# Optimization experiments

Hardware: AMD Instinct MI355X
Metric: run time of the kernel (lower is better)

Reference implementation:

```python
import jax, jax.numpy as jnp
import numpy as np

N_NODES = 79
RAW_FEAT = 26
D_IN = RAW_FEAT + 6      # 32, in_channels after position concat
D_OUT = 2 * D_IN         # 64, out_channel_fac * in_channels
HIDDEN = 256
N_EDGES = 3000
BATCH = 256
POS_IDX = [120,124,128,132,136,140,144,148,152,237,241,245,249,253,257,261,265,269,354,358,362,366,370,374,378,382,386,471,475,479,483,487,491,495,499,503,588,592,596,600,604,608,612,616,620,705,709,713,717,721,725,729,733,737,822,826,830,834,838,842,846,850,854,48,53,60,67,73,157,352,388,583,586,817,901,906,913,920,926]


def _positions():
    width, height = 39, 25
    p = np.asarray(POS_IDX)
    xn = (p % width) / (width - 1)
    yn = (p // width) / (height - 1)
    feats = np.stack([xn, yn,
                      (np.sin(xn * 2 * np.pi) + 1) / 2,
                      (np.cos(xn * 2 * np.pi) + 1) / 2,
                      (np.sin(yn * 2 * np.pi) + 1) / 2,
                      (np.cos(yn * 2 * np.pi) + 1) / 2], axis=-1)
    return jnp.asarray(feats, jnp.float32)


def setup_inputs() -> dict:
    key = jax.random.key(0)
    ks = jax.random.split(key, 20)
    s = 0.05
    inp = {
        "state": jax.random.normal(ks[0], (BATCH, N_NODES, RAW_FEAT), jnp.float32),
        "pos_feat": _positions(),
        "edge_weights": jax.random.uniform(ks[1], (N_EDGES, 1), jnp.float32),
        # TransformerConv params (heads=1, edge_dim=1): torch Linear weights [out,in]
        "Wq": jax.random.normal(ks[2], (D_OUT, D_IN)) * s, "bq": jnp.zeros((D_OUT,)),
        "Wk": jax.random.normal(ks[3], (D_OUT, D_IN)) * s, "bk": jnp.zeros((D_OUT,)),
        "Wv": jax.random.normal(ks[4], (D_OUT, D_IN)) * s, "bv": jnp.zeros((D_OUT,)),
        "We": jax.random.normal(ks[5], (D_OUT, 1)) * s,            # lin_edge, bias=False
        "Wskip": jax.random.normal(ks[6], (D_OUT, D_IN)) * s, "bskip": jnp.zeros((D_OUT,)),
        # MLP head
        "W1": jax.random.normal(ks[7], (HIDDEN, D_IN + D_OUT + 1)) * s, "b1": jnp.zeros((HIDDEN,)),
        "g1": jnp.ones((HIDDEN,)), "beta1": jnp.zeros((HIDDEN,)),
        "W2": jax.random.normal(ks[8], (HIDDEN, HIDDEN)) * s, "b2": jnp.zeros((HIDDEN,)),
        "g2": jnp.ones((HIDDEN,)), "beta2": jnp.zeros((HIDDEN,)),
        "W3": jax.random.normal(ks[9], (1, HIDDEN)) * s, "b3": jnp.zeros((1,)),
        "edge_index": jax.random.randint(ks[10], (2, N_EDGES), 0, N_NODES, jnp.int32),
    }
    return inp


def _layernorm(x, g, b):
    m = x.mean(-1, keepdims=True)
    v = ((x - m) ** 2).mean(-1, keepdims=True)
    return (x - m) / jnp.sqrt(v + 1e-5) * g + b


def reference(state, pos_feat, edge_weights, Wq, bq, Wk, bk, Wv, bv, We, Wskip, bskip,
              W1, b1, g1, beta1, W2, b2, g2, beta2, W3, b3, edge_index):
    B = state.shape[0]
    # concat normalized positional features (shared across batch)
    x = jnp.concatenate([state, jnp.broadcast_to(pos_feat, (B, N_NODES, 6))], -1)  # [B,N,D_IN]
    src, dst = edge_index[0], edge_index[1]
    e = edge_weights @ We.T  # [E, D_OUT] edge embedding, shared across batch
    scale = 1.0 / jnp.sqrt(jnp.float32(D_OUT))

    def conv_one(xg):  # TransformerConv, heads=1, concat, root_weight
        q = xg @ Wq.T + bq
        k = xg @ Wk.T + bk
        v = xg @ Wv.T + bv
        ke = k[src] + e                      # [E, D_OUT]
        ve = v[src] + e
        alpha = (q[dst] * ke).sum(-1) * scale  # [E]
        amax = jax.ops.segment_max(alpha, dst, num_segments=N_NODES)
        amax = jnp.where(jnp.isfinite(amax), amax, 0.0)
        ex = jnp.exp(alpha - amax[dst])
        den = jax.ops.segment_sum(ex, dst, num_segments=N_NODES)
        w = ex / (den[dst] + 1e-16)
        agg = jax.ops.segment_sum(ve * w[:, None], dst, num_segments=N_NODES)
        return agg + xg @ Wskip.T + bskip

    out1 = jax.nn.relu(jax.vmap(conv_one)(x))  # [B,N,D_OUT]
    total_agents = x[..., 1].sum(-1)[:, None, None]  # [B,1,1]
    h = jnp.concatenate([out1, jnp.broadcast_to(total_agents, (B, N_NODES, 1)), x], -1)
    h = jax.nn.leaky_relu(_layernorm(h @ W1.T + b1, g1, beta1))
    h = jax.nn.leaky_relu(_layernorm(h @ W2.T + b2, g2, beta2))
    conc = jax.nn.softplus(h @ W3.T + b3).squeeze(-1)  # [B,N]
    action = conc / (conc.sum(-1, keepdims=True) + 1e-20)  # deterministic path
    return action
```

## Files before the change

### kernel.cpp

```cpp
#include <hip/hip_runtime.h>
#include <hip/hip_bf16.h>

#define N_NODES 79
#define RAW_FEAT 26
#define D_IN 32
#define D_OUT 64
#define HIDDEN 256
#define N_EDGES 3000
#define BATCH 256
#define M_ROWS (BATCH * N_NODES)
#define K1PAD 112

__global__ __launch_bounds__(256) void k_prep(
    const float* __restrict__ W1, const float* __restrict__ W2,
    const int* __restrict__ ei, const float* __restrict__ ew,
    float* __restrict__ W1t, float* __restrict__ W2t,
    int* __restrict__ rp, int* __restrict__ csr_src,
    int* __restrict__ csr_dst, float* __restrict__ csr_ew)
{
    __shared__ float tile[64][65];
    __shared__ int cnt[N_NODES];
    __shared__ int base[N_NODES + 1];
    const int tid = threadIdx.x, bid = blockIdx.x;

    if (bid < 24) {
        const float* in; float* out; int C, Kpad, kb, rb;
        if (bid < 8) { in = W1; out = W1t; C = 97; Kpad = K1PAD;
                       kb = (bid & 1) * 64; rb = (bid >> 1) * 64; }
        else         { int b = bid - 8; in = W2; out = W2t; C = 256; Kpad = 256;
                       kb = (b & 3) * 64; rb = (b >> 2) * 64; }
        for (int i = tid; i < 4096; i += 256) {
            int rr = i >> 6, kk = i & 63;
            int r = rb + rr, k = kb + kk;
            tile[rr][kk] = (k < C) ? in[r * C + k] : 0.f;
        }
        __syncthreads();
        for (int i = tid; i < 4096; i += 256) {
            int kk = i >> 6, rr = i & 63;
            int k = kb + kk, r = rb + rr;
            if (k < Kpad) out[(size_t)k * HIDDEN + r] = tile[rr][kk];
        }
        return;
    }

    if (tid < N_NODES) cnt[tid] = 0;
    __syncthreads();
    for (int e = tid; e < N_EDGES; e += 256) atomicAdd(&cnt[ei[N_EDGES + e]], 1);
    __syncthreads();
    if (tid == 0) {
        int run = 0;
        for (int n = 0; n < N_NODES; ++n) { base[n] = run; run += cnt[n]; }
        base[N_NODES] = run;
    }
    __syncthreads();
    if (tid < N_NODES + 1) rp[tid] = base[tid];
    if (tid < N_NODES) cnt[tid] = base[tid];
    __syncthreads();
    for (int e = tid; e < N_EDGES; e += 256) {
        int d = ei[N_EDGES + e];
        int p = atomicAdd(&cnt[d], 1);
        csr_src[p] = ei[e];
        csr_dst[p] = d;
        csr_ew[p]  = ew[e];
    }
}

#define DOT4(S, Aa, Bb) S += Aa.x * Bb.x + Aa.y * Bb.y + Aa.z * Bb.z + Aa.w * Bb.w;

__global__ __launch_bounds__(512) void k1_conv(
    const float* __restrict__ state, const float* __restrict__ pos,
    const int* __restrict__ rp_g, const int* __restrict__ csrc_g,
    const int* __restrict__ cdst_g, const float* __restrict__ cew_g,
    const float* __restrict__ Wq, const float* __restrict__ bq,
    const float* __restrict__ Wk, const float* __restrict__ bk,
    const float* __restrict__ Wv, const float* __restrict__ bv,
    const float* __restrict__ We, const float* __restrict__ Wsk,
    const float* __restrict__ bsk,
    float* __restrict__ out1_ws, float* __restrict__ ta_ws)
{
    __shared__ __align__(16) float qs [80 * 68];
    __shared__ __align__(16) float kss[80 * 68];
    __shared__ __align__(16) float vss[80 * 68];
    __shared__ __align__(16) float o1s[N_NODES * 68];
    __shared__ __align__(16) float xs[N_NODES * 32];
    __shared__ __align__(16) float SA[80 * 80];
    __shared__ __align__(16) float alpha[N_EDGES];
    __shared__ __align__(16) float ewc[N_EDGES];
    __shared__ unsigned short srcs[N_EDGES], dsts[N_EDGES];
    __shared__ __align__(16) float eW[64];
    __shared__ int   rp_s[80];
    __shared__ float qWe[80], csum_s[80];

    const int b = blockIdx.x, tid = threadIdx.x;

    for (int t = tid; t < N_NODES * 32; t += 512) {
        int n = t >> 5, c = t & 31;
        xs[t] = (c < RAW_FEAT) ? state[(b * N_NODES + n) * RAW_FEAT + c]
                               : pos[n * 6 + (c - RAW_FEAT)];
    }
    for (int t = tid; t < N_EDGES; t += 512) {
        srcs[t] = (unsigned short)csrc_g[t];
        dsts[t] = (unsigned short)cdst_g[t];
        ewc[t]  = cew_g[t];
    }
    if (tid < 64) eW[tid] = We[tid];
    if (tid < 80) rp_s[tid] = rp_g[tid];
    for (int t = tid; t < 68; t += 512) {
        qs[79 * 68 + t] = 0.f; kss[79 * 68 + t] = 0.f; vss[79 * 68 + t] = 0.f;
    }
    __syncthreads();

    {
        const float4* xs4 = (const float4*)xs;
        const float4* Wq4 = (const float4*)Wq;
        const float4* Wk4 = (const float4*)Wk;
        const float4* Wv4 = (const float4*)Wv;
        const float4* Ws4 = (const float4*)Wsk;
        for (int t = tid; t < N_NODES * 64; t += 512) {
            int n = t >> 6, d = t & 63;
            float aq = bq[d], ak = bk[d], av = bv[d], ask = bsk[d];
            #pragma unroll
            for (int c4 = 0; c4 < 8; ++c4) {
                float4 xv = xs4[n * 8 + c4];
                float4 wq = Wq4[d * 8 + c4];
                float4 wk = Wk4[d * 8 + c4];
                float4 wv = Wv4[d * 8 + c4];
                float4 wsv = Ws4[d * 8 + c4];
                DOT4(aq, xv, wq)
                DOT4(ak, xv, wk)
                DOT4(av, xv, wv)
                DOT4(ask, xv, wsv)
            }
            qs [n * 68 + d] = aq;
            kss[n * 68 + d] = ak;
            vss[n * 68 + d] = av;
            o1s[n * 68 + d] = ask;
        }
        if (tid == 511) {
            float s = 0.f;
            #pragma unroll
            for (int n = 0; n < N_NODES; ++n) s += xs[n * 32 + 1];
            ta_ws[b] = s;
        }
    }
    __syncthreads();

    if (tid < N_NODES) {
        const float4* q4 = (const float4*)(qs + tid * 68);
        const float4* e4 = (const float4*)eW;
        float s = 0.f;
        #pragma unroll
        for (int i = 0; i < 16; ++i) {
            float4 a = q4[i], e = e4[i];
            DOT4(s, a, e)
        }
        qWe[tid] = s;
    }
    __syncthreads();

    {
        const int rg = tid >> 5, cgp = tid & 31;
        const int r0 = rg * 5;
        int c0 = cgp * 3; if (c0 > 76) c0 = 76;
        float s00 = 0, s01 = 0, s02 = 0;
        float s10 = 0, s11 = 0, s12 = 0;
        float s20 = 0, s21 = 0, s22 = 0;
        float s30 = 0, s31 = 0, s32 = 0;
        float s40 = 0, s41 = 0, s42 = 0;
        const float4* q4p = (const float4*)qs;
        const float4* k4p = (const float4*)kss;
        for (int k4 = 0; k4 < 16; ++k4) {
            float4 q0 = q4p[(r0 + 0) * 17 + k4];
            float4 q1 = q4p[(r0 + 1) * 17 + k4];
            float4 q2 = q4p[(r0 + 2) * 17 + k4];
            float4 q3 = q4p[(r0 + 3) * 17 + k4];
            float4 q4v = q4p[(r0 + 4) * 17 + k4];
            float4 c0v = k4p[(c0 + 0) * 17 + k4];
            float4 c1v = k4p[(c0 + 1) * 17 + k4];
            float4 c2v = k4p[(c0 + 2) * 17 + k4];
            DOT4(s00, q0, c0v)  DOT4(s01, q0, c1v)  DOT4(s02, q0, c2v)
            DOT4(s10, q1, c0v)  DOT4(s11, q1, c1v)  DOT4(s12, q1, c2v)
            DOT4(s20, q2, c0v)  DOT4(s21, q2, c1v)  DOT4(s22, q2, c2v)
            DOT4(s30, q3, c0v)  DOT4(s31, q3, c1v)  DOT4(s32, q3, c2v)
            DOT4(s40, q4v, c0v) DOT4(s41, q4v, c1v) DOT4(s42, q4v, c2v)
        }
        SA[(r0 + 0) * 80 + c0 + 0] = s00; SA[(r0 + 0) * 80 + c0 + 1] = s01; SA[(r0 + 0) * 80 + c0 + 2] = s02;
        SA[(r0 + 1) * 80 + c0 + 0] = s10; SA[(r0 + 1) * 80 + c0 + 1] = s11; SA[(r0 + 1) * 80 + c0 + 2] = s12;
        SA[(r0 + 2) * 80 + c0 + 0] = s20; SA[(r0 + 2) * 80 + c0 + 1] = s21; SA[(r0 + 2) * 80 + c0 + 2] = s22;
        SA[(r0 + 3) * 80 + c0 + 0] = s30; SA[(r0 + 3) * 80 + c0 + 1] = s31; SA[(r0 + 3) * 80 + c0 + 2] = s32;
        SA[(r0 + 4) * 80 + c0 + 0] = s40; SA[(r0 + 4) * 80 + c0 + 1] = s41; SA[(r0 + 4) * 80 + c0 + 2] = s42;
    }
    __syncthreads();

    for (int t = tid; t < N_EDGES; t += 512) {
        int s = srcs[t], d = dsts[t];
        alpha[t] = 0.125f * (SA[d * 80 + s] + ewc[t] * qWe[d]);
    }
    __syncthreads();

    for (int t = tid; t < 6400; t += 512) SA[t] = 0.f;
    __syncthreads();

    if (tid < N_NODES) {
        int e0 = rp_s[tid], e1 = rp_s[tid + 1];
        float m = -1e30f;
        for (int e = e0; e < e1; ++e) m = fmaxf(m, alpha[e]);
        float s = 0.f, cs = 0.f;
        for (int e = e0; e < e1; ++e) {
            float ex = expf(alpha[e] - m);
            alpha[e] = ex;
            s += ex; cs += ex * ewc[e];
        }
        float rden = 1.f / (s + 1e-16f);
        csum_s[tid] = cs * rden;
        float* Ar = SA + tid * 80;
        for (int e = e0; e < e1; ++e) Ar[srcs[e]] += alpha[e] * rden;
    }
    __syncthreads();

    {
        const int rowg = tid >> 4, colg = tid & 15;
        int n0 = rowg * 3; if (n0 > 76) n0 = 76;
        float4 g0 = {0.f, 0.f, 0.f, 0.f};
        float4 g1 = {0.f, 0.f, 0.f, 0.f};
        float4 g2 = {0.f, 0.f, 0.f, 0.f};
        const float4* A4  = (const float4*)SA;
        const float4* v4p = (const float4*)vss;

#define AGGSTEP(COMP, SS) { \
        float4 vv = v4p[(s4 * 4 + SS) * 17 + colg]; \
        g0.x += a0.COMP * vv.x; g0.y += a0.COMP * vv.y; g0.z += a0.COMP * vv.z; g0.w += a0.COMP * vv.w; \
        g1.x += a1.COMP * vv.x; g1.y += a1.COMP * vv.y; g1.z += a1.COMP * vv.z; g1.w += a1.COMP * vv.w; \
        g2.x += a2.COMP * vv.x; g2.y += a2.COMP * vv.y; g2.z += a2.COMP * vv.z; g2.w += a2.COMP * vv.w; }

        for (int s4 = 0; s4 < 20; ++s4) {
            float4 a0 = A4[(n0 + 0) * 20 + s4];
            float4 a1 = A4[(n0 + 1) * 20 + s4];
            float4 a2 = A4[(n0 + 2) * 20 + s4];
            AGGSTEP(x, 0)
            AGGSTEP(y, 1)
            AGGSTEP(z, 2)
            AGGSTEP(w, 3)
        }
#undef AGGSTEP

        const float4* o4 = (const float4*)o1s;
        const float4* e4 = (const float4*)eW;
        float4 ev = e4[colg];

#define AGGOUT(GI, I) { int n = n0 + I; if (n < N_NODES) { \
        float4 sk = o4[n * 17 + colg]; float cs = csum_s[n]; float4 r; \
        r.x = fmaxf(sk.x + GI.x + cs * ev.x, 0.f); \
        r.y = fmaxf(sk.y + GI.y + cs * ev.y, 0.f); \
        r.z = fmaxf(sk.z + GI.z + cs * ev.z, 0.f); \
        r.w = fmaxf(sk.w + GI.w + cs * ev.w, 0.f); \
        ((float4*)out1_ws)[((size_t)b * N_NODES + n) * 16 + colg] = r; } }

        AGGOUT(g0, 0)
        AGGOUT(g1, 1)
        AGGOUT(g2, 2)
#undef AGGOUT
    }
}

__global__ __launch_bounds__(256, 4) void k23_mlp(
    const float* __restrict__ state, const float* __restrict__ pos,
    const float* __restrict__ out1_ws, const float* __restrict__ ta_ws,
    const float* __restrict__ W1t, const float* __restrict__ b1,
    const float* __restrict__ g1, const float* __restrict__ be1,
    const float* __restrict__ W2t, const float* __restrict__ b2,
    const float* __restrict__ g2, const float* __restrict__ be2,
    const float* __restrict__ W3, const float* __restrict__ b3,
    float* __restrict__ conc_ws)
{
    __shared__ __align__(16) float A1[16 * K1PAD];
    __shared__ __align__(16) float A2[16 * 256];
    __shared__ __align__(16) float Ws[16 * 256];

    const int tid = threadIdx.x;
    const int lane = tid & 63;
    const int wv = tid >> 6;
    const int m0 = blockIdx.x * 16;

    const float4* W1t4 = (const float4*)W1t;
    const float4* W2t4 = (const float4*)W2t;
    const float4* A1r4 = (const float4*)A1;
    const float4* A2r4 = (const float4*)A2;
    float4* Ws4 = (float4*)Ws;
    const float4* Wsc4 = (const float4*)Ws;

    for (int t = tid; t < 16 * K1PAD; t += 256) {
        int r = t / K1PAD, k = t - r * K1PAD;
        int m = m0 + r;
        float v = 0.f;
        if (k < 64)       v = out1_ws[m * 64 + k];
        else if (k == 64) v = ta_ws[m / N_NODES];
        else if (k < 91)  v = state[m * RAW_FEAT + (k - 65)];
        else if (k < 97)  { int n = m - (m / N_NODES) * N_NODES;
                            v = pos[n * 6 + (k - 91)]; }
        A1[t] = v;
    }

    float4 pre0 = W1t4[(wv + 0) * 64 + lane];
    float4 pre1 = W1t4[(wv + 4) * 64 + lane];
    float4 pre2 = W1t4[(wv + 8) * 64 + lane];
    float4 pre3 = W1t4[(wv + 12) * 64 + lane];
    __syncthreads();

    float4 acc0 = {0.f, 0.f, 0.f, 0.f};
    float4 acc1 = {0.f, 0.f, 0.f, 0.f};
    float4 acc2 = {0.f, 0.f, 0.f, 0.f};
    float4 acc3 = {0.f, 0.f, 0.f, 0.f};

#define GSTEP(COMP, WIDX) { \
    float4 w = Wsc4[(kq * 4 + WIDX) * 64 + lane]; \
    acc0.x += a0.COMP * w.x; acc0.y += a0.COMP * w.y; acc0.z += a0.COMP * w.z; acc0.w += a0.COMP * w.w; \
    acc1.x += a1.COMP * w.x; acc1.y += a1.COMP * w.y; acc1.z += a1.COMP * w.z; acc1.w += a1.COMP * w.w; \
    acc2.x += a2.COMP * w.x; acc2.y += a2.COMP * w.y; acc2.z += a2.COMP * w.z; acc2.w += a2.COMP * w.w; \
    acc3.x += a3.COMP * w.x; acc3.y += a3.COMP * w.y; acc3.z += a3.COMP * w.z; acc3.w += a3.COMP * w.w; }

    for (int ch = 0; ch < 7; ++ch) {
        Ws4[(wv + 0) * 64 + lane] = pre0;
        Ws4[(wv + 4) * 64 + lane] = pre1;
        Ws4[(wv + 8) * 64 + lane] = pre2;
        Ws4[(wv + 12) * 64 + lane] = pre3;
        __syncthreads();
        if (ch < 6) {
            pre0 = W1t4[((ch + 1) * 16 + wv + 0) * 64 + lane];
            pre1 = W1t4[((ch + 1) * 16 + wv + 4) * 64 + lane];
            pre2 = W1t4[((ch + 1) * 16 + wv + 8) * 64 + lane];
            pre3 = W1t4[((ch + 1) * 16 + wv + 12) * 64 + lane];
        }
        #pragma unroll
        for (int kq = 0; kq < 4; ++kq) {
            float4 a0 = A1r4[(4 * wv + 0) * 28 + ch * 4 + kq];
            float4 a1 = A1r4[(4 * wv + 1) * 28 + ch * 4 + kq];
            float4 a2 = A1r4[(4 * wv + 2) * 28 + ch * 4 + kq];
            float4 a3 = A1r4[(4 * wv + 3) * 28 + ch * 4 + kq];
            GSTEP(x, 0)
            GSTEP(y, 1)
            GSTEP(z, 2)
            GSTEP(w, 3)
        }
        __syncthreads();
    }

    pre0 = W2t4[(wv + 0) * 64 + lane];
    pre1 = W2t4[(wv + 4) * 64 + lane];
    pre2 = W2t4[(wv + 8) * 64 + lane];
    pre3 = W2t4[(wv + 12) * 64 + lane];

    {
        float4 bv = ((const float4*)b1)[lane];
        float4 gv = ((const float4*)g1)[lane];
        float4 ev = ((const float4*)be1)[lane];

#define LN1_ROW(ACC, RR) { \
        float v0 = ACC.x + bv.x, v1 = ACC.y + bv.y, v2 = ACC.z + bv.z, v3 = ACC.w + bv.w; \
        float sm = v0 + v1 + v2 + v3, sq = v0 * v0 + v1 * v1 + v2 * v2 + v3 * v3; \
        for (int off = 32; off >= 1; off >>= 1) { sm += __shfl_xor(sm, off, 64); sq += __shfl_xor(sq, off, 64); } \
        float mu = sm * (1.f / 256.f), rstd = rsqrtf(sq * (1.f / 256.f) - mu * mu + 1e-5f); \
        float4 yv; \
        yv.x = (v0 - mu) * rstd * gv.x + ev.x; yv.y = (v1 - mu) * rstd * gv.y + ev.y; \
        yv.z = (v2 - mu) * rstd * gv.z + ev.z; yv.w = (v3 - mu) * rstd * gv.w + ev.w; \
        yv.x = yv.x > 0.f ? yv.x : 0.01f * yv.x; yv.y = yv.y > 0.f ? yv.y : 0.01f * yv.y; \
        yv.z = yv.z > 0.f ? yv.z : 0.01f * yv.z; yv.w = yv.w > 0.f ? yv.w : 0.01f * yv.w; \
        ((float4*)A2)[(4 * wv + RR) * 64 + lane] = yv; }

        LN1_ROW(acc0, 0)
        LN1_ROW(acc1, 1)
        LN1_ROW(acc2, 2)
        LN1_ROW(acc3, 3)
#undef LN1_ROW
        acc0 = {0.f, 0.f, 0.f, 0.f};
        acc1 = {0.f, 0.f, 0.f, 0.f};
        acc2 = {0.f, 0.f, 0.f, 0.f};
        acc3 = {0.f, 0.f, 0.f, 0.f};
    }
    __syncthreads();

    for (int ch = 0; ch < 16; ++ch) {
        Ws4[(wv + 0) * 64 + lane] = pre0;
        Ws4[(wv + 4) * 64 + lane] = pre1;
        Ws4[(wv + 8) * 64 + lane] = pre2;
        Ws4[(wv + 12) * 64 + lane] = pre3;
        __syncthreads();
        if (ch < 15) {
            pre0 = W2t4[((ch + 1) * 16 + wv + 0) * 64 + lane];
            pre1 = W2t4[((ch + 1) * 16 + wv + 4) * 64 + lane];
            pre2 = W2t4[((ch + 1) * 16 + wv + 8) * 64 + lane];
            pre3 = W2t4[((ch + 1) * 16 + wv + 12) * 64 + lane];
        }
        #pragma unroll
        for (int kq = 0; kq < 4; ++kq) {
            float4 a0 = A2r4[(4 * wv + 0) * 64 + ch * 4 + kq];
            float4 a1 = A2r4[(4 * wv + 1) * 64 + ch * 4 + kq];
            float4 a2 = A2r4[(4 * wv + 2) * 64 + ch * 4 + kq];
            float4 a3 = A2r4[(4 * wv + 3) * 64 + ch * 4 + kq];
            GSTEP(x, 0)
            GSTEP(y, 1)
            GSTEP(z, 2)
            GSTEP(w, 3)
        }
        __syncthreads();
    }
#undef GSTEP

    {
        float4 bv = ((const float4*)b2)[lane];
        float4 gv = ((const float4*)g2)[lane];
        float4 ev = ((const float4*)be2)[lane];
        float4 w3 = ((const float4*)W3)[lane];
        float bb3 = b3[0];

#define LN2_ROW(ACC, RR) { \
        float v0 = ACC.x + bv.x, v1 = ACC.y + bv.y, v2 = ACC.z + bv.z, v3 = ACC.w + bv.w; \
        float sm = v0 + v1 + v2 + v3, sq = v0 * v0 + v1 * v1 + v2 * v2 + v3 * v3; \
        for (int off = 32; off >= 1; off >>= 1) { sm += __shfl_xor(sm, off, 64); sq += __shfl_xor(sq, off, 64); } \
        float mu = sm * (1.f / 256.f), rstd = rsqrtf(sq * (1.f / 256.f) - mu * mu + 1e-5f); \
        float z0 = (v0 - mu) * rstd * gv.x + ev.x, z1 = (v1 - mu) * rstd * gv.y + ev.y; \
        float z2 = (v2 - mu) * rstd * gv.z + ev.z, z3 = (v3 - mu) * rstd * gv.w + ev.w; \
        z0 = z0 > 0.f ? z0 : 0.01f * z0; z1 = z1 > 0.f ? z1 : 0.01f * z1; \
        z2 = z2 > 0.f ? z2 : 0.01f * z2; z3 = z3 > 0.f ? z3 : 0.01f * z3; \
        float part = z0 * w3.x + z1 * w3.y + z2 * w3.z + z3 * w3.w; \
        for (int off = 32; off >= 1; off >>= 1) part += __shfl_xor(part, off, 64); \
        if (lane == 0) { float x = part + bb3; \
            conc_ws[m0 + 4 * wv + RR] = fmaxf(x, 0.f) + log1pf(expf(-fabsf(x))); } }

        LN2_ROW(acc0, 0)
        LN2_ROW(acc1, 1)
        LN2_ROW(acc2, 2)
        LN2_ROW(acc3, 3)
#undef LN2_ROW
    }
}

__global__ __launch_bounds__(128) void k4_norm(
    const float* __restrict__ conc_ws, float* __restrict__ out)
{
    __shared__ float red[128];
    const int b = blockIdx.x, tid = threadIdx.x;
    float v = 0.f;
    if (tid < N_NODES) v = conc_ws[b * N_NODES + tid];
    red[tid] = v;
    __syncthreads();
    for (int off = 64; off >= 1; off >>= 1) {
        if (tid < off) red[tid] += red[tid + off];
        __syncthreads();
    }
    float s = red[0];
    if (tid < N_NODES) out[b * N_NODES + tid] = v / (s + 1e-20f);
}

extern "C" void kernel_launch(void* const* d_in, const int* in_sizes, int n_in,
                              void* d_out, int out_size, void* d_ws, size_t ws_size,
                              hipStream_t stream) {
    const float* state = (const float*)d_in[0];
    const float* pos   = (const float*)d_in[1];
    const float* ew    = (const float*)d_in[2];
    const float* Wq  = (const float*)d_in[3];  const float* bq  = (const float*)d_in[4];
    const float* Wk  = (const float*)d_in[5];  const float* bk  = (const float*)d_in[6];
    const float* Wv  = (const float*)d_in[7];  const float* bv  = (const float*)d_in[8];
    const float* We  = (const float*)d_in[9];
    const float* Wsk = (const float*)d_in[10]; const float* bsk = (const float*)d_in[11];
    const float* W1  = (const float*)d_in[12]; const float* b1  = (const float*)d_in[13];
    const float* g1  = (const float*)d_in[14]; const float* be1 = (const float*)d_in[15];
    const float* W2  = (const float*)d_in[16]; const float* b2  = (const float*)d_in[17];
    const float* g2  = (const float*)d_in[18]; const float* be2 = (const float*)d_in[19];
    const float* W3  = (const float*)d_in[20]; const float* b3  = (const float*)d_in[21];
    const int*   ei  = (const int*)d_in[22];

    float* ws   = (float*)d_ws;
    float* ta   = ws;
    float* out1 = ws + 256;
    float* conc = out1 + (size_t)M_ROWS * 64;
    float* W1t  = conc + M_ROWS;
    float* W2t  = W1t + K1PAD * HIDDEN;
    int*   rp   = (int*)(W2t + HIDDEN * HIDDEN);
    int*   csrc = rp + 80;
    int*   cdst = csrc + N_EDGES;
    float* cew  = (float*)(cdst + N_EDGES);
    float* out  = (float*)d_out;

    k_prep<<<dim3(25), dim3(256), 0, stream>>>(
        W1, W2, ei, ew, W1t, W2t, rp, csrc, cdst, cew);
    k1_conv<<<dim3(BATCH), dim3(512), 0, stream>>>(
        state, pos, rp, csrc, cdst, cew,
        Wq, bq, Wk, bk, Wv, bv, We, Wsk, bsk, out1, ta);
    k23_mlp<<<dim3(M_ROWS / 16), dim3(256), 0, stream>>>(
        state, pos, out1, ta, W1t, b1, g1, be1,
        W2t, b2, g2, be2, W3, b3, conc);
    k4_norm<<<dim3(BATCH), dim3(128), 0, stream>>>(conc, out);
}
```

Measured before the change: 246.5 us.

## Split QKV projection into register-tiled GEMM kernel and widen MLP row tile

Adds a k_prep block that packs Wq/Wk/Wv/Wskip and their biases into one transposed 32x256 matrix. A new k_qkv kernel computes all four projections as a register-tiled GEMM and writes them to a workspace buffer. k1_conv now loads those projections instead of computing per-thread dot products, and reduces total_agents with a parallel tree instead of a single thread. k23_mlp now processes 32 rows per block, with each thread computing 8 columns for 4 rows, which halves how often the weights are reloaded per row. The cost is an extra kernel launch, a round trip of about 20 MB through global memory for qkvs, and higher LDS and register use per block, which may lower occupancy.

```diff
diff --git a/kernel.cpp b/kernel.cpp
--- a/kernel.cpp
+++ b/kernel.cpp
@@ -14,7 +14,12 @@
 __global__ __launch_bounds__(256) void k_prep(
     const float* __restrict__ W1, const float* __restrict__ W2,
     const int* __restrict__ ei, const float* __restrict__ ew,
+    const float* __restrict__ Wq, const float* __restrict__ Wk,
+    const float* __restrict__ Wv, const float* __restrict__ Wsk,
+    const float* __restrict__ bq, const float* __restrict__ bk,
+    const float* __restrict__ bv, const float* __restrict__ bsk,
     float* __restrict__ W1t, float* __restrict__ W2t,
+    float* __restrict__ Wall_t, float* __restrict__ ball,
     int* __restrict__ rp, int* __restrict__ csr_src,
     int* __restrict__ csr_dst, float* __restrict__ csr_ew)
 {
@@ -43,6 +48,25 @@
         return;
     }
 
+    if (bid == 25) {
+        for (int t = tid; t < 32 * 256; t += 256) {
+            int k = t >> 8, j = t & 255;
+            float v;
+            if (j < 64)       v = Wq [j * 32 + k];
+            else if (j < 128) v = Wk [(j - 64) * 32 + k];
+            else if (j < 192) v = Wv [(j - 128) * 32 + k];
+            else              v = Wsk[(j - 192) * 32 + k];
+            Wall_t[t] = v;
+        }
+        if (tid < 64) {
+            ball[tid]       = bq[tid];
+            ball[64 + tid]  = bk[tid];
+            ball[128 + tid] = bv[tid];
+            ball[192 + tid] = bsk[tid];
+        }
+        return;
+    }
+
     if (tid < N_NODES) cnt[tid] = 0;
     __syncthreads();
     for (int e = tid; e < N_EDGES; e += 256) atomicAdd(&cnt[ei[N_EDGES + e]], 1);
@@ -67,22 +91,91 @@
 
 #define DOT4(S, Aa, Bb) S += Aa.x * Bb.x + Aa.y * Bb.y + Aa.z * Bb.z + Aa.w * Bb.w;
 
+__global__ __launch_bounds__(256) void k_qkv(
+    const float* __restrict__ state, const float* __restrict__ pos,
+    const float* __restrict__ Wall_t, const float* __restrict__ ball,
+    float* __restrict__ qkvs)
+{
+    __shared__ __align__(16) float Ax[32 * 32];
+    __shared__ __align__(16) float Ws[32 * 256];
+
+    const int tid = threadIdx.x;
+    const int cg = tid & 31;
+    const int rg = tid >> 5;
+    const int m0 = blockIdx.x * 32;
+
+    for (int t = tid; t < 32 * 32; t += 256) {
+        int r = t >> 5, k = t & 31;
+        int m = m0 + r, n = m - (m / N_NODES) * N_NODES;
+        Ax[t] = (k < RAW_FEAT) ? state[m * RAW_FEAT + k] : pos[n * 6 + (k - RAW_FEAT)];
+    }
+    {
+        const float4* Wg4 = (const float4*)Wall_t;
+        float4* Ws4w = (float4*)Ws;
+        #pragma unroll
+        for (int i = 0; i < 8; ++i) Ws4w[tid + 256 * i] = Wg4[tid + 256 * i];
+    }
+    __syncthreads();
+
+    float4 accL0 = {0,0,0,0}, accL1 = {0,0,0,0}, accL2 = {0,0,0,0}, accL3 = {0,0,0,0};
+    float4 accH0 = {0,0,0,0}, accH1 = {0,0,0,0}, accH2 = {0,0,0,0}, accH3 = {0,0,0,0};
+    const float4* Ax4 = (const float4*)Ax;
+    const float4* Ws4 = (const float4*)Ws;
+
+#define QSTEP(COMP, KS) { \
+    float4 wL = Ws4[(kq * 4 + KS) * 64 + cg]; \
+    float4 wH = Ws4[(kq * 4 + KS) * 64 + 32 + cg]; \
+    accL0.x += a0.COMP * wL.x; accL0.y += a0.COMP * wL.y; accL0.z += a0.COMP * wL.z; accL0.w += a0.COMP * wL.w; \
+    accL1.x += a1.COMP * wL.x; accL1.y += a1.COMP * wL.y; accL1.z += a1.COMP * wL.z; accL1.w += a1.COMP * wL.w; \
+    accL2.x += a2.COMP * wL.x; accL2.y += a2.COMP * wL.y; accL2.z += a2.COMP * wL.z; accL2.w += a2.COMP * wL.w; \
+    accL3.x += a3.COMP * wL.x; accL3.y += a3.COMP * wL.y; accL3.z += a3.COMP * wL.z; accL3.w += a3.COMP * wL.w; \
+    accH0.x += a0.COMP * wH.x; accH0.y += a0.COMP * wH.y; accH0.z += a0.COMP * wH.z; accH0.w += a0.COMP * wH.w; \
+    accH1.x += a1.COMP * wH.x; accH1.y += a1.COMP * wH.y; accH1.z += a1.COMP * wH.z; accH1.w += a1.COMP * wH.w; \
+    accH2.x += a2.COMP * wH.x; accH2.y += a2.COMP * wH.y; accH2.z += a2.COMP * wH.z; accH2.w += a2.COMP * wH.w; \
+    accH3.x += a3.COMP * wH.x; accH3.y += a3.COMP * wH.y; accH3.z += a3.COMP * wH.z; accH3.w += a3.COMP * wH.w; }
+
+    #pragma unroll
+    for (int kq = 0; kq < 8; ++kq) {
+        float4 a0 = Ax4[(rg * 4 + 0) * 8 + kq];
+        float4 a1 = Ax4[(rg * 4 + 1) * 8 + kq];
+        float4 a2 = Ax4[(rg * 4 + 2) * 8 + kq];
+        float4 a3 = Ax4[(rg * 4 + 3) * 8 + kq];
+        QSTEP(x, 0)
+        QSTEP(y, 1)
+        QSTEP(z, 2)
+        QSTEP(w, 3)
+    }
+#undef QSTEP
+
+    {
+        float4 bL = ((const float4*)ball)[cg];
+        float4 bH = ((const float4*)ball)[32 + cg];
+        float4* o4 = (float4*)qkvs;
+#define QOUT(ACCL, ACCH, RR) { \
+        float4 vL, vH; \
+        vL.x = ACCL.x + bL.x; vL.y = ACCL.y + bL.y; vL.z = ACCL.z + bL.z; vL.w = ACCL.w + bL.w; \
+        vH.x = ACCH.x + bH.x; vH.y = ACCH.y + bH.y; vH.z = ACCH.z + bH.z; vH.w = ACCH.w + bH.w; \
+        o4[(size_t)(m0 + rg * 4 + RR) * 64 + cg] = vL; \
+        o4[(size_t)(m0 + rg * 4 + RR) * 64 + 32 + cg] = vH; }
+        QOUT(accL0, accH0, 0)
+        QOUT(accL1, accH1, 1)
+        QOUT(accL2, accH2, 2)
+        QOUT(accL3, accH3, 3)
+#undef QOUT
+    }
+}
+
 __global__ __launch_bounds__(512) void k1_conv(
-    const float* __restrict__ state, const float* __restrict__ pos,
+    const float* __restrict__ state, const float* __restrict__ qkvs,
     const int* __restrict__ rp_g, const int* __restrict__ csrc_g,
     const int* __restrict__ cdst_g, const float* __restrict__ cew_g,
-    const float* __restrict__ Wq, const float* __restrict__ bq,
-    const float* __restrict__ Wk, const float* __restrict__ bk,
-    const float* __restrict__ Wv, const float* __restrict__ bv,
-    const float* __restrict__ We, const float* __restrict__ Wsk,
-    const float* __restrict__ bsk,
+    const float* __restrict__ We,
     float* __restrict__ out1_ws, float* __restrict__ ta_ws)
 {
     __shared__ __align__(16) float qs [80 * 68];
     __shared__ __align__(16) float kss[80 * 68];
     __shared__ __align__(16) float vss[80 * 68];
     __shared__ __align__(16) float o1s[N_NODES * 68];
-    __shared__ __align__(16) float xs[N_NODES * 32];
     __shared__ __align__(16) float SA[80 * 80];
     __shared__ __align__(16) float alpha[N_EDGES];
     __shared__ __align__(16) float ewc[N_EDGES];
@@ -90,13 +183,20 @@
     __shared__ __align__(16) float eW[64];
     __shared__ int   rp_s[80];
     __shared__ float qWe[80], csum_s[80];
+    __shared__ float red80[80];
 
     const int b = blockIdx.x, tid = threadIdx.x;
 
-    for (int t = tid; t < N_NODES * 32; t += 512) {
-        int n = t >> 5, c = t & 31;
-        xs[t] = (c < RAW_FEAT) ? state[(b * N_NODES + n) * RAW_FEAT + c]
-                               : pos[n * 6 + (c - RAW_FEAT)];
+    {
+        const float4* qk4 = (const float4*)qkvs;
+        for (int t = tid; t < N_NODES * 64; t += 512) {
+            int n = t >> 6, j = t & 63;
+            float4 v = qk4[(size_t)(b * N_NODES + n) * 64 + j];
+            if (j < 16)      ((float4*)qs )[n * 17 + j]        = v;
+            else if (j < 32) ((float4*)kss)[n * 17 + (j - 16)] = v;
+            else if (j < 48) ((float4*)vss)[n * 17 + (j - 32)] = v;
+            else             ((float4*)o1s)[n * 17 + (j - 48)] = v;
+        }
     }
     for (int t = tid; t < N_EDGES; t += 512) {
         srcs[t] = (unsigned short)csrc_g[t];
@@ -105,45 +205,18 @@
     }
     if (tid < 64) eW[tid] = We[tid];
     if (tid < 80) rp_s[tid] = rp_g[tid];
+    if (tid < 79) red80[tid] = state[(b * N_NODES + tid) * RAW_FEAT + 1];
+    if (tid == 79) red80[79] = 0.f;
     for (int t = tid; t < 68; t += 512) {
         qs[79 * 68 + t] = 0.f; kss[79 * 68 + t] = 0.f; vss[79 * 68 + t] = 0.f;
     }
     __syncthreads();
 
-    {
-        const float4* xs4 = (const float4*)xs;
-        const float4* Wq4 = (const float4*)Wq;
-        const float4* Wk4 = (const float4*)Wk;
-        const float4* Wv4 = (const float4*)Wv;
-        const float4* Ws4 = (const float4*)Wsk;
-        for (int t = tid; t < N_NODES * 64; t += 512) {
-            int n = t >> 6, d = t & 63;
-            float aq = bq[d], ak = bk[d], av = bv[d], ask = bsk[d];
-            #pragma unroll
-            for (int c4 = 0; c4 < 8; ++c4) {
-                float4 xv = xs4[n * 8 + c4];
-                float4 wq = Wq4[d * 8 + c4];
-                float4 wk = Wk4[d * 8 + c4];
-                float4 wv = Wv4[d * 8 + c4];
-                float4 wsv = Ws4[d * 8 + c4];
-                DOT4(aq, xv, wq)
-                DOT4(ak, xv, wk)
-                DOT4(av, xv, wv)
-                DOT4(ask, xv, wsv)
-            }
-            qs [n * 68 + d] = aq;
-            kss[n * 68 + d] = ak;
-            vss[n * 68 + d] = av;
-            o1s[n * 68 + d] = ask;
-        }
-        if (tid == 511) {
-            float s = 0.f;
-            #pragma unroll
-            for (int n = 0; n < N_NODES; ++n) s += xs[n * 32 + 1];
-            ta_ws[b] = s;
-        }
-    }
-    __syncthreads();
+    for (int off = 64; off >= 1; off >>= 1) {
+        if (tid < off && tid + off < 80) red80[tid] += red80[tid + off];
+        __syncthreads();
+    }
+    if (tid == 0) ta_ws[b] = red80[0];
 
     if (tid < N_NODES) {
         const float4* q4 = (const float4*)(qs + tid * 68);
@@ -263,7 +336,7 @@
     }
 }
 
-__global__ __launch_bounds__(256, 4) void k23_mlp(
+__global__ __launch_bounds__(256) void k23_mlp(
     const float* __restrict__ state, const float* __restrict__ pos,
     const float* __restrict__ out1_ws, const float* __restrict__ ta_ws,
     const float* __restrict__ W1t, const float* __restrict__ b1,
@@ -273,23 +346,23 @@
     const float* __restrict__ W3, const float* __restrict__ b3,
     float* __restrict__ conc_ws)
 {
-    __shared__ __align__(16) float A1[16 * K1PAD];
-    __shared__ __align__(16) float A2[16 * 256];
+    __shared__ __align__(16) float A1[32 * K1PAD];
+    __shared__ __align__(16) float A2[32 * 256];
     __shared__ __align__(16) float Ws[16 * 256];
 
     const int tid = threadIdx.x;
-    const int lane = tid & 63;
-    const int wv = tid >> 6;
-    const int m0 = blockIdx.x * 16;
+    const int cg = tid & 31;
+    const int rg = tid >> 5;
+    const int m0 = blockIdx.x * 32;
 
     const float4* W1t4 = (const float4*)W1t;
     const float4* W2t4 = (const float4*)W2t;
-    const float4* A1r4 = (const float4*)A1;
-    const float4* A2r4 = (const float4*)A2;
-    float4* Ws4 = (float4*)Ws;
-    const float4* Wsc4 = (const float4*)Ws;
-
-    for (int t = tid; t < 16 * K1PAD; t += 256) {
+    const float4* A1_4 = (const float4*)A1;
+    const float4* A2_4 = (const float4*)A2;
+    float4* Ws4w = (float4*)Ws;
+    const float4* Ws4 = (const float4*)Ws;
+
+    for (int t = tid; t < 32 * K1PAD; t += 256) {
         int r = t / K1PAD, k = t - r * K1PAD;
         int m = m0 + r;
         float v = 0.f;
@@ -300,137 +373,146 @@
                             v = pos[n * 6 + (k - 91)]; }
         A1[t] = v;
     }
-
-    float4 pre0 = W1t4[(wv + 0) * 64 + lane];
-    float4 pre1 = W1t4[(wv + 4) * 64 + lane];
-    float4 pre2 = W1t4[(wv + 8) * 64 + lane];
-    float4 pre3 = W1t4[(wv + 12) * 64 + lane];
-    __syncthreads();
-
-    float4 acc0 = {0.f, 0.f, 0.f, 0.f};
-    float4 acc1 = {0.f, 0.f, 0.f, 0.f};
-    float4 acc2 = {0.f, 0.f, 0.f, 0.f};
-    float4 acc3 = {0.f, 0.f, 0.f, 0.f};
-
-#define GSTEP(COMP, WIDX) { \
-    float4 w = Wsc4[(kq * 4 + WIDX) * 64 + lane]; \
-    acc0.x += a0.COMP * w.x; acc0.y += a0.COMP * w.y; acc0.z += a0.COMP * w.z; acc0.w += a0.COMP * w.w; \
-    acc1.x += a1.COMP * w.x; acc1.y += a1.COMP * w.y; acc1.z += a1.COMP * w.z; acc1.w += a1.COMP * w.w; \
-    acc2.x += a2.COMP * w.x; acc2.y += a2.COMP * w.y; acc2.z += a2.COMP * w.z; acc2.w += a2.COMP * w.w; \
-    acc3.x += a3.COMP * w.x; acc3.y += a3.COMP * w.y; acc3.z += a3.COMP * w.z; acc3.w += a3.COMP * w.w; }
+    float4 pre0 = W1t4[tid];
+    float4 pre1 = W1t4[tid + 256];
+    float4 pre2 = W1t4[tid + 512];
+    float4 pre3 = W1t4[tid + 768];
+    __syncthreads();
+
+    float4 accL0 = {0,0,0,0}, accL1 = {0,0,0,0}, accL2 = {0,0,0,0}, accL3 = {0,0,0,0};
+    float4 accH0 = {0,0,0,0}, accH1 = {0,0,0,0}, accH2 = {0,0,0,0}, accH3 = {0,0,0,0};
+
+#define KSTEP(COMP, KS) { \
+    float4 wL = Ws4[(kq * 4 + KS) * 64 + cg]; \
+    float4 wH = Ws4[(kq * 4 + KS) * 64 + 32 + cg]; \
+    accL0.x += a0.COMP * wL.x; accL0.y += a0.COMP * wL.y; accL0.z += a0.COMP * wL.z; accL0.w += a0.COMP * wL.w; \
+    accL1.x += a1.COMP * wL.x; accL1.y += a1.COMP * wL.y; accL1.z += a1.COMP * wL.z; accL1.w += a1.COMP * wL.w; \
+    accL2.x += a2.COMP * wL.x; accL2.y += a2.COMP * wL.y; accL2.z += a2.COMP * wL.z; accL2.w += a2.COMP * wL.w; \
+    accL3.x += a3.COMP * wL.x; accL3.y += a3.COMP * wL.y; accL3.z += a3.COMP * wL.z; accL3.w += a3.COMP * wL.w; \
+    accH0.x += a0.COMP * wH.x; accH0.y += a0.COMP * wH.y; accH0.z += a0.COMP * wH.z; accH0.w += a0.COMP * wH.w; \
+    accH1.x += a1.COMP * wH.x; accH1.y += a1.COMP * wH.y; accH1.z += a1.COMP * wH.z; accH1.w += a1.COMP * wH.w; \
+    accH2.x += a2.COMP * wH.x; accH2.y += a2.COMP * wH.y; accH2.z += a2.COMP * wH.z; accH2.w += a2.COMP * wH.w; \
+    accH3.x += a3.COMP * wH.x; accH3.y += a3.COMP * wH.y; accH3.z += a3.COMP * wH.z; accH3.w += a3.COMP * wH.w; }
 
     for (int ch = 0; ch < 7; ++ch) {
-        Ws4[(wv + 0) * 64 + lane] = pre0;
-        Ws4[(wv + 4) * 64 + lane] = pre1;
-        Ws4[(wv + 8) * 64 + lane] = pre2;
-        Ws4[(wv + 12) * 64 + lane] = pre3;
+        Ws4w[tid] = pre0; Ws4w[tid + 256] = pre1;
+        Ws4w[tid + 512] = pre2; Ws4w[tid + 768] = pre3;
         __syncthreads();
         if (ch < 6) {
-            pre0 = W1t4[((ch + 1) * 16 + wv + 0) * 64 + lane];
-            pre1 = W1t4[((ch + 1) * 16 + wv + 4) * 64 + lane];
-            pre2 = W1t4[((ch + 1) * 16 + wv + 8) * 64 + lane];
-            pre3 = W1t4[((ch + 1) * 16 + wv + 12) * 64 + lane];
+            pre0 = W1t4[(ch + 1) * 1024 + tid];
+            pre1 = W1t4[(ch + 1) * 1024 + tid + 256];
+            pre2 = W1t4[(ch + 1) * 1024 + tid + 512];
+            pre3 = W1t4[(ch + 1) * 1024 + tid + 768];
+        } else {
+            pre0 = W2t4[tid];
+            pre1 = W2t4[tid + 256];
+            pre2 = W2t4[tid + 512];
+            pre3 = W2t4[tid + 768];
         }
         #pragma unroll
         for (int kq = 0; kq < 4; ++kq) {
-            float4 a0 = A1r4[(4 * wv + 0) * 28 + ch * 4 + kq];
-            float4 a1 = A1r4[(4 * wv + 1) * 28 + ch * 4 + kq];
-            float4 a2 = A1r4[(4 * wv + 2) * 28 + ch * 4 + kq];
-            float4 a3 = A1r4[(4 * wv + 3) * 28 + ch * 4 + kq];
-            GSTEP(x, 0)
-            GSTEP(y, 1)
-            GSTEP(z, 2)
-            GSTEP(w, 3)
-        }
-        __syncthreads();
-    }
-
-    pre0 = W2t4[(wv + 0) * 64 + lane];
-    pre1 = W2t4[(wv + 4) * 64 + lane];
-    pre2 = W2t4[(wv + 8) * 64 + lane];
-    pre3 = W2t4[(wv + 12) * 64 + lane];
-
-    {
-        float4 bv = ((const float4*)b1)[lane];
-        float4 gv = ((const float4*)g1)[lane];
-        float4 ev = ((const float4*)be1)[lane];
-
-#define LN1_ROW(ACC, RR) { \
-        float v0 = ACC.x + bv.x, v1 = ACC.y + bv.y, v2 = ACC.z + bv.z, v3 = ACC.w + bv.w; \
-        float sm = v0 + v1 + v2 + v3, sq = v0 * v0 + v1 * v1 + v2 * v2 + v3 * v3; \
-        for (int off = 32; off >= 1; off >>= 1) { sm += __shfl_xor(sm, off, 64); sq += __shfl_xor(sq, off, 64); } \
+            float4 a0 = A1_4[(rg * 4 + 0) * 28 + ch * 4 + kq];
+            float4 a1 = A1_4[(rg * 4 + 1) * 28 + ch * 4 + kq];
+            float4 a2 = A1_4[(rg * 4 + 2) * 28 + ch * 4 + kq];
+            float4 a3 = A1_4[(rg * 4 + 3) * 28 + ch * 4 + kq];
+            KSTEP(x, 0)
+            KSTEP(y, 1)
+            KSTEP(z, 2)
+            KSTEP(w, 3)
+        }
+        __syncthreads();
+    }
+
+    {
+        float4 bL = ((const float4*)b1)[cg],  bH = ((const float4*)b1)[32 + cg];
+        float4 gL = ((const float4*)g1)[cg],  gH = ((const float4*)g1)[32 + cg];
+        float4 eL = ((const float4*)be1)[cg], eH = ((const float4*)be1)[32 + cg];
+
+#define LN1_ROW(AL, AH, RR) { \
+        float v0 = AL.x + bL.x, v1 = AL.y + bL.y, v2 = AL.z + bL.z, v3 = AL.w + bL.w; \
+        float v4 = AH.x + bH.x, v5 = AH.y + bH.y, v6 = AH.z + bH.z, v7 = AH.w + bH.w; \
+        float sm = v0 + v1 + v2 + v3 + v4 + v5 + v6 + v7; \
+        float sq = v0*v0 + v1*v1 + v2*v2 + v3*v3 + v4*v4 + v5*v5 + v6*v6 + v7*v7; \
+        for (int off = 16; off >= 1; off >>= 1) { sm += __shfl_xor(sm, off, 64); sq += __shfl_xor(sq, off, 64); } \
         float mu = sm * (1.f / 256.f), rstd = rsqrtf(sq * (1.f / 256.f) - mu * mu + 1e-5f); \
-        float4 yv; \
-        yv.x = (v0 - mu) * rstd * gv.x + ev.x; yv.y = (v1 - mu) * rstd * gv.y + ev.y; \
-        yv.z = (v2 - mu) * rstd * gv.z + ev.z; yv.w = (v3 - mu) * rstd * gv.w + ev.w; \
-        yv.x = yv.x > 0.f ? yv.x : 0.01f * yv.x; yv.y = yv.y > 0.f ? yv.y : 0.01f * yv.y; \
-        yv.z = yv.z > 0.f ? yv.z : 0.01f * yv.z; yv.w = yv.w > 0.f ? yv.w : 0.01f * yv.w; \
-        ((float4*)A2)[(4 * wv + RR) * 64 + lane] = yv; }
-
-        LN1_ROW(acc0, 0)
-        LN1_ROW(acc1, 1)
-        LN1_ROW(acc2, 2)
-        LN1_ROW(acc3, 3)
+        float4 yL, yH; \
+        yL.x = (v0 - mu) * rstd * gL.x + eL.x; yL.y = (v1 - mu) * rstd * gL.y + eL.y; \
+        yL.z = (v2 - mu) * rstd * gL.z + eL.z; yL.w = (v3 - mu) * rstd * gL.w + eL.w; \
+        yH.x = (v4 - mu) * rstd * gH.x + eH.x; yH.y = (v5 - mu) * rstd * gH.y + eH.y; \
+        yH.z = (v6 - mu) * rstd * gH.z + eH.z; yH.w = (v7 - mu) * rstd * gH.w + eH.w; \
+        yL.x = yL.x > 0.f ? yL.x : 0.01f * yL.x; yL.y = yL.y > 0.f ? yL.y : 0.01f * yL.y; \
+        yL.z = yL.z > 0.f ? yL.z : 0.01f * yL.z; yL.w = yL.w > 0.f ? yL.w : 0.01f * yL.w; \
+        yH.x = yH.x > 0.f ? yH.x : 0.01f * yH.x; yH.y = yH.y > 0.f ? yH.y : 0.01f * yH.y; \
+        yH.z = yH.z > 0.f ? yH.z : 0.01f * yH.z; yH.w = yH.w > 0.f ? yH.w : 0.01f * yH.w; \
+        ((float4*)A2)[(rg * 4 + RR) * 64 + cg] = yL; \
+        ((float4*)A2)[(rg * 4 + RR) * 64 + 32 + cg] = yH; }
+
+        LN1_ROW(accL0, accH0, 0)
+        LN1_ROW(accL1, accH1, 1)
+        LN1_ROW(accL2, accH2, 2)
+        LN1_ROW(accL3, accH3, 3)
 #undef LN1_ROW
-        acc0 = {0.f, 0.f, 0.f, 0.f};
-        acc1 = {0.f, 0.f, 0.f, 0.f};
-        acc2 = {0.f, 0.f, 0.f, 0.f};
-        acc3 = {0.f, 0.f, 0.f, 0.f};
-    }
-    __syncthreads();
+        accL0 = {0,0,0,0}; accL1 = {0,0,0,0}; accL2 = {0,0,0,0}; accL3 = {0,0,0,0};
+        accH0 = {0,0,0,0}; accH1 = {0,0,0,0}; accH2 = {0,0,0,0}; accH3 = {0,0,0,0};
+    }
 
     for (int ch = 0; ch < 16; ++ch) {
-        Ws4[(wv + 0) * 64 + lane] = pre0;
-        Ws4[(wv + 4) * 64 + lane] = pre1;
-        Ws4[(wv + 8) * 64 + lane] = pre2;
-        Ws4[(wv + 12) * 64 + lane] = pre3;
+        Ws4w[tid] = pre0; Ws4w[tid + 256] = pre1;
+        Ws4w[tid + 512] = pre2; Ws4w[tid + 768] = pre3;
         __syncthreads();
         if (ch < 15) {
-            pre0 = W2t4[((ch + 1) * 16 + wv + 0) * 64 + lane];
-            pre1 = W2t4[((ch + 1) * 16 + wv + 4) * 64 + lane];
-            pre2 = W2t4[((ch + 1) * 16 + wv + 8) * 64 + lane];
-            pre3 = W2t4[((ch + 1) * 16 + wv + 12) * 64 + lane];
+            pre0 = W2t4[(ch + 1) * 1024 + tid];
+            pre1 = W2t4[(ch + 1) * 1024 + tid + 256];
+            pre2 = W2t4[(ch + 1) * 1024 + tid + 512];
+            pre3 = W2t4[(ch + 1) * 1024 + tid + 768];
         }
         #pragma unroll
         for (int kq = 0; kq < 4; ++kq) {
-            float4 a0 = A2r4[(4 * wv + 0) * 64 + ch * 4 + kq];
-            float4 a1 = A2r4[(4 * wv + 1) * 64 + ch * 4 + kq];
-            float4 a2 = A2r4[(4 * wv + 2) * 64 + ch * 4 + kq];
-            float4 a3 = A2r4[(4 * wv + 3) * 64 + ch * 4 + kq];
-            GSTEP(x, 0)
-            GSTEP(y, 1)
-            GSTEP(z, 2)
-            GSTEP(w, 3)
-        }
-        __syncthreads();
-    }
-#undef GSTEP
-
-    {
-        float4 bv = ((const float4*)b2)[lane];
-        float4 gv = ((const float4*)g2)[lane];
-        float4 ev = ((const float4*)be2)[lane];
-        float4 w3 = ((const float4*)W3)[lane];
+            float4 a0 = A2_4[(rg * 4 + 0) * 64 + ch * 4 + kq];
+            float4 a1 = A2_4[(rg * 4 + 1) * 64 + ch * 4 + kq];
+            float4 a2 = A2_4[(rg * 4 + 2) * 64 + ch * 4 + kq];
+            float4 a3 = A2_4[(rg * 4 + 3) * 64 + ch * 4 + kq];
+            KSTEP(x, 0)
+            KSTEP(y, 1)
+            KSTEP(z, 2)
+            KSTEP(w, 3)
+        }
+        __syncthreads();
+    }
+#undef KSTEP
+
+    {
+        float4 bL = ((const float4*)b2)[cg],  bH = ((const float4*)b2)[32 + cg];
+        float4 gL = ((const float4*)g2)[cg],  gH = ((const float4*)g2)[32 + cg];
+        float4 eL = ((const float4*)be2)[cg], eH = ((const float4*)be2)[32 + cg];
+        float4 wL3 = ((const float4*)W3)[cg], wH3 = ((const float4*)W3)[32 + cg];
         float bb3 = b3[0];
 
-#define LN2_ROW(ACC, RR) { \
-        float v0 = ACC.x + bv.x, v1 = ACC.y + bv.y, v2 = ACC.z + bv.z, v3 = ACC.w + bv.w; \
-        float sm = v0 + v1 + v2 + v3, sq = v0 * v0 + v1 * v1 + v2 * v2 + v3 * v3; \
-        for (int off = 32; off >= 1; off >>= 1) { sm += __shfl_xor(sm, off, 64); sq += __shfl_xor(sq, off, 64); } \
+#define LN2_ROW(AL, AH, RR) { \
+        float v0 = AL.x + bL.x, v1 = AL.y + bL.y, v2 = AL.z + bL.z, v3 = AL.w + bL.w; \
+        float v4 = AH.x + bH.x, v5 = AH.y + bH.y, v6 = AH.z + bH.z, v7 = AH.w + bH.w; \
+        float sm = v0 + v1 + v2 + v3 + v4 + v5 + v6 + v7; \
+        float sq = v0*v0 + v1*v1 + v2*v2 + v3*v3 + v4*v4 + v5*v5 + v6*v6 + v7*v7; \
+        for (int off = 16; off >= 1; off >>= 1) { sm += __shfl_xor(sm, off, 64); sq += __shfl_xor(sq, off, 64); } \
         float mu = sm * (1.f / 256.f), rstd = rsqrtf(sq * (1.f / 256.f) - mu * mu + 1e-5f); \
-        float z0 = (v0 - mu) * rstd * gv.x + ev.x, z1 = (v1 - mu) * rstd * gv.y + ev.y; \
-        float z2 = (v2 - mu) * rstd * gv.z + ev.z, z3 = (v3 - mu) * rstd * gv.w + ev.w; \
+        float z0 = (v0 - mu) * rstd * gL.x + eL.x, z1 = (v1 - mu) * rstd * gL.y + eL.y; \
+        float z2 = (v2 - mu) * rstd * gL.z + eL.z, z3 = (v3 - mu) * rstd * gL.w + eL.w; \
+        float z4 = (v4 - mu) * rstd * gH.x + eH.x, z5 = (v5 - mu) * rstd * gH.y + eH.y; \
+        float z6 = (v6 - mu) * rstd * gH.z + eH.z, z7 = (v7 - mu) * rstd * gH.w + eH.w; \
         z0 = z0 > 0.f ? z0 : 0.01f * z0; z1 = z1 > 0.f ? z1 : 0.01f * z1; \
         z2 = z2 > 0.f ? z2 : 0.01f * z2; z3 = z3 > 0.f ? z3 : 0.01f * z3; \
-        float part = z0 * w3.x + z1 * w3.y + z2 * w3.z + z3 * w3.w; \
-        for (int off = 32; off >= 1; off >>= 1) part += __shfl_xor(part, off, 64); \
-        if (lane == 0) { float x = part + bb3; \
-            conc_ws[m0 + 4 * wv + RR] = fmaxf(x, 0.f) + log1pf(expf(-fabsf(x))); } }
-
-        LN2_ROW(acc0, 0)
-        LN2_ROW(acc1, 1)
-        LN2_ROW(acc2, 2)
-        LN2_ROW(acc3, 3)
+        z4 = z4 > 0.f ? z4 : 0.01f * z4; z5 = z5 > 0.f ? z5 : 0.01f * z5; \
+        z6 = z6 > 0.f ? z6 : 0.01f * z6; z7 = z7 > 0.f ? z7 : 0.01f * z7; \
+        float part = z0 * wL3.x + z1 * wL3.y + z2 * wL3.z + z3 * wL3.w \
+                   + z4 * wH3.x + z5 * wH3.y + z6 * wH3.z + z7 * wH3.w; \
+        for (int off = 16; off >= 1; off >>= 1) part += __shfl_xor(part, off, 64); \
+        if (cg == 0) { float x = part + bb3; \
+            conc_ws[m0 + rg * 4 + RR] = fmaxf(x, 0.f) + log1pf(expf(-fabsf(x))); } }
+
+        LN2_ROW(accL0, accH0, 0)
+        LN2_ROW(accL1, accH1, 1)
+        LN2_ROW(accL2, accH2, 2)
+        LN2_ROW(accL3, accH3, 3)
 #undef LN2_ROW
     }
 }
@@ -470,24 +552,29 @@
     const float* W3  = (const float*)d_in[20]; const float* b3  = (const float*)d_in[21];
     const int*   ei  = (const int*)d_in[22];
 
-    float* ws   = (float*)d_ws;
-    float* ta   = ws;
-    float* out1 = ws + 256;
-    float* conc = out1 + (size_t)M_ROWS * 64;
-    float* W1t  = conc + M_ROWS;
-    float* W2t  = W1t + K1PAD * HIDDEN;
-    int*   rp   = (int*)(W2t + HIDDEN * HIDDEN);
-    int*   csrc = rp + 80;
-    int*   cdst = csrc + N_EDGES;
-    float* cew  = (float*)(cdst + N_EDGES);
-    float* out  = (float*)d_out;
-
-    k_prep<<<dim3(25), dim3(256), 0, stream>>>(
-        W1, W2, ei, ew, W1t, W2t, rp, csrc, cdst, cew);
+    float* ws    = (float*)d_ws;
+    float* ta    = ws;
+    float* out1  = ws + 256;
+    float* conc  = out1 + (size_t)M_ROWS * 64;
+    float* W1t   = conc + M_ROWS;
+    float* W2t   = W1t + K1PAD * HIDDEN;
+    float* Wall  = W2t + HIDDEN * HIDDEN;
+    float* ball  = Wall + 32 * 256;
+    float* qkvs  = ball + 256;
+    int*   rp    = (int*)(qkvs + (size_t)M_ROWS * 256);
+    int*   csrc  = rp + 80;
+    int*   cdst  = csrc + N_EDGES;
+    float* cew   = (float*)(cdst + N_EDGES);
+    float* out   = (float*)d_out;
+
+    k_prep<<<dim3(26), dim3(256), 0, stream>>>(
+        W1, W2, ei, ew, Wq, Wk, Wv, Wsk, bq, bk, bv, bsk,
+        W1t, W2t, Wall, ball, rp, csrc, cdst, cew);
+    k_qkv<<<dim3(M_ROWS / 32), dim3(256), 0, stream>>>(
+        state, pos, Wall, ball, qkvs);
     k1_conv<<<dim3(BATCH), dim3(512), 0, stream>>>(
-        state, pos, rp, csrc, cdst, cew,
-        Wq, bq, Wk, bk, Wv, bv, We, Wsk, bsk, out1, ta);
-    k23_mlp<<<dim3(M_ROWS / 16), dim3(256), 0, stream>>>(
+        state, qkvs, rp, csrc, cdst, cew, We, out1, ta);
+    k23_mlp<<<dim3(M_ROWS / 32), dim3(256), 0, stream>>>(
         state, pos, out1, ta, W1t, b1, g1, be1,
         W2t, b2, g2, be2, W3, b3, conc);
     k4_norm<<<dim3(BATCH), dim3(128), 0, stream>>>(conc, out);
```

After: 235.5 us. 1.05x faster.
